# Kernel tuning notes

Hardware: AMD Instinct MI355X
Metric: run time of the kernel (lower is better)

Reference implementation:

```python
import jax, jax.numpy as jnp
import numpy as np

N_USERS = 200_000
N_ITEMS = 100_000
EMB = 64
N_EDGES = 5_000_000
N_LAYERS = 3


def setup_inputs() -> dict:
    key = jax.random.key(0)
    k1, k2, k3, k4, k5 = jax.random.split(key, 5)
    emb_user = jax.random.normal(k1, (N_USERS, EMB), dtype=jnp.float32) * 0.1
    emb_item = jax.random.normal(k2, (N_ITEMS, EMB), dtype=jnp.float32) * 0.1
    n_nodes = N_USERS + N_ITEMS
    edge_row = jax.random.randint(k3, (N_EDGES,), 0, n_nodes, dtype=jnp.int32)
    edge_col = jax.random.randint(k4, (N_EDGES,), 0, n_nodes, dtype=jnp.int32)
    # normalized adjacency values (positive, < 1), stand-in for D^-1/2 A D^-1/2
    edge_val = jax.random.uniform(k5, (N_EDGES,), dtype=jnp.float32)
    return {"emb_user": emb_user, "emb_item": emb_item,
            "edge_val": edge_val, "edge_row": edge_row, "edge_col": edge_col}


def reference(emb_user, emb_item, edge_val, edge_row, edge_col):
    n_users = emb_user.shape[0]
    n_nodes = n_users + emb_item.shape[0]
    # 0th-layer embedding matrix: cat(user, item)  [N, D]
    x = jnp.concatenate([emb_user, emb_item], axis=0)
    layers = [x]
    for _ in range(N_LAYERS):
        # SpMM: out[r] += val * x[c] for each edge (r, c)
        x = jax.ops.segment_sum(edge_val[:, None] * x[edge_col], edge_row,
                                num_segments=n_nodes)
        layers.append(x)
    # layer combination: mean over all layers
    agg = jnp.mean(jnp.stack(layers, axis=0), axis=0)
    return agg[:n_users], agg[n_users:]
```

## Files before the change

### kernel.cpp

```cpp
#include <hip/hip_runtime.h>

#define N_USERS 200000
#define N_ITEMS 100000
#define N_NODES 300000
#define EMB     64
#define N_EDGES 5000000

typedef float f32x4 __attribute__((ext_vector_type(4)));
typedef _Float16 f16;
typedef f16 f16x4 __attribute__((ext_vector_type(4)));

struct alignas(8) SRec { unsigned int rc; float val; };

#define BSHIFT 10
#define BROWS  (1 << BSHIFT)
#define NBUCK  ((N_NODES + BROWS - 1) >> BSHIFT)
#define CAP    20000
#define BIN_CHUNK 16384
#define COLMASK 0x7FFFFu
#define INIT_BLOCKS 2048

__global__ __launch_bounds__(256) void fused_init_bin_kernel(
    const float* __restrict__ user, const float* __restrict__ item,
    f16* __restrict__ x0,
    const int4* __restrict__ row4, const int4* __restrict__ col4,
    const float4* __restrict__ val4,
    int* __restrict__ bcursor, SRec* __restrict__ stage, int bin_blocks)
{
    int t = threadIdx.x;
    if ((int)blockIdx.x < bin_blocks) {
        __shared__ int hist[NBUCK];
        __shared__ int base_[NBUCK];
        const int Q = N_EDGES / 4;
        long q0 = (long)blockIdx.x * (BIN_CHUNK / 4);

        for (int k = t; k < NBUCK; k += 256) hist[k] = 0;
        __syncthreads();

        int4 ra[16];
        const bool full = (q0 + (BIN_CHUNK / 4) <= Q);
        if (full) {
            #pragma unroll
            for (int k = 0; k < 16; ++k)
                ra[k] = row4[q0 + k * 256 + t];
            #pragma unroll
            for (int k = 0; k < 16; ++k) {
                atomicAdd(&hist[ra[k].x >> BSHIFT], 1);
                atomicAdd(&hist[ra[k].y >> BSHIFT], 1);
                atomicAdd(&hist[ra[k].z >> BSHIFT], 1);
                atomicAdd(&hist[ra[k].w >> BSHIFT], 1);
            }
        } else {
            #pragma unroll
            for (int k = 0; k < 16; ++k) {
                long q = q0 + k * 256 + t;
                if (q < Q) {
                    ra[k] = row4[q];
                    atomicAdd(&hist[ra[k].x >> BSHIFT], 1);
                    atomicAdd(&hist[ra[k].y >> BSHIFT], 1);
                    atomicAdd(&hist[ra[k].z >> BSHIFT], 1);
                    atomicAdd(&hist[ra[k].w >> BSHIFT], 1);
                }
            }
        }
        __syncthreads();
        for (int k = t; k < NBUCK; k += 256) {
            int h = hist[k];
            base_[k] = h ? atomicAdd(&bcursor[k], h) : 0;
            hist[k] = 0;
        }
        __syncthreads();
        #pragma unroll
        for (int g = 0; g < 4; ++g) {
            int4 c4[4]; float4 v4[4];
            #pragma unroll
            for (int j = 0; j < 4; ++j) {
                long q = q0 + (g * 4 + j) * 256 + t;
                if (q < Q) { c4[j] = col4[q]; v4[j] = val4[q]; }
            }
            #pragma unroll
            for (int j = 0; j < 4; ++j) {
                long q = q0 + (g * 4 + j) * 256 + t;
                if (q < Q) {
                    int4 r = ra[g * 4 + j];
                    int   rr[4] = {r.x, r.y, r.z, r.w};
                    int   cc[4] = {c4[j].x, c4[j].y, c4[j].z, c4[j].w};
                    float vv[4] = {v4[j].x, v4[j].y, v4[j].z, v4[j].w};
                    #pragma unroll
                    for (int m = 0; m < 4; ++m) {
                        int b   = rr[m] >> BSHIFT;
                        int pos = base_[b] + atomicAdd(&hist[b], 1);
                        SRec s;
                        s.rc  = ((unsigned)(rr[m] & (BROWS - 1)) << 19)
                              | (unsigned)cc[m];
                        s.val = vv[m];
                        stage[(size_t)b * CAP + pos] = s;
                    }
                }
            }
        }
    } else {
        const int nu4 = N_USERS * EMB / 4;
        const int nt4 = N_NODES * EMB / 4;
        int i0 = ((int)blockIdx.x - bin_blocks) * 256 + t;
        const int stride = INIT_BLOCKS * 256;
        for (int i = i0; i < nt4; i += stride) {
            float4 vv = (i < nu4) ? reinterpret_cast<const float4*>(user)[i]
                                  : reinterpret_cast<const float4*>(item)[i - nu4];
            f16x4 hx = {(f16)vv.x, (f16)vv.y, (f16)vv.z, (f16)vv.w};
            reinterpret_cast<f16x4*>(x0)[i] = hx;
        }
    }
}

__global__ __launch_bounds__(1024) void bucket_scan_scatter_kernel(
    const SRec* __restrict__ stage, const int* __restrict__ bsize,
    int* __restrict__ start, int* __restrict__ pcol, f16* __restrict__ pval)
{
    __shared__ int sizes[NBUCK];
    __shared__ int cur[BROWS];
    __shared__ int sc[1024];
    __shared__ int lcol[CAP];
    __shared__ f16 lval[CAP];
    __shared__ int sbase;

    int b    = blockIdx.x;
    int t    = threadIdx.x;
    int row0 = b << BSHIFT;
    int rows = N_NODES - row0; if (rows > BROWS) rows = BROWS;

    if (t < NBUCK) sizes[t] = bsize[t];
    cur[t] = 0;
    __syncthreads();
    if (t == 0) {
        int s = 0;
        for (int k = 0; k < b; ++k) s += sizes[k];
        sbase = s;
    }
    __syncthreads();
    const int  base = sbase;
    const int  size = sizes[b];
    const SRec* seg = stage + (size_t)b * CAP;

    for (int e = t; e < size; e += 1024)
        atomicAdd(&cur[seg[e].rc >> 19], 1);
    __syncthreads();

    int a = cur[t];
    sc[t] = a;
    __syncthreads();
    for (int ofs = 1; ofs < 1024; ofs <<= 1) {
        int v = (t >= ofs) ? sc[t - ofs] : 0;
        __syncthreads();
        sc[t] += v;
        __syncthreads();
    }
    int excl = sc[t] - a;
    cur[t] = excl;
    if (t < rows) start[row0 + t] = base + excl;
    if (b == NBUCK - 1 && t == 0) start[N_NODES] = N_EDGES;
    __syncthreads();

    for (int e = t; e < size; e += 1024) {
        SRec srec = seg[e];
        int idx = atomicAdd(&cur[srec.rc >> 19], 1);
        lcol[idx] = (int)(srec.rc & COLMASK);
        lval[idx] = (f16)srec.val;
    }
    __syncthreads();

    for (int i = t; i < size; i += 1024) pcol[base + i] = lcol[i];
    for (int i = t; i < size; i += 1024) pval[base + i] = lval[i];
}

__global__ __launch_bounds__(256, 4) void spmm_csr_kernel(
    const f16* __restrict__ x, const int* __restrict__ pcol,
    const f16* __restrict__ pval, const int* __restrict__ start,
    f16* __restrict__ y,
    const f16* __restrict__ xa, const f16* __restrict__ xb,
    float* __restrict__ out, int mode)
{
    int g = blockIdx.x * (256 / 16) + (threadIdx.x >> 4);
    if (g >= N_NODES) return;
    const int lane16 = threadIdx.x & 15;
    const int d      = lane16 * 4;
    const int gbase  = threadIdx.x & 48;

    int beg = start[g];
    int end = start[g + 1];
    float4 acc = {0.f, 0.f, 0.f, 0.f};

    for (int jb = beg; jb < end; jb += 16) {
        int   mycol = 0; float myval = 0.f;
        if (jb + lane16 < end) {
            mycol = pcol[jb + lane16];
            myval = (float)pval[jb + lane16];
        }

        int   cols[16];
        float vals[16];
        #pragma unroll
        for (int k = 0; k < 16; ++k) {
            cols[k] = __shfl(mycol, gbase + k, 64);
            vals[k] = __shfl(myval, gbase + k, 64);
        }

        f16x4 xv[16];
        #pragma unroll
        for (int k = 0; k < 16; ++k) {
            xv[k] = *reinterpret_cast<const f16x4*>(
                x + (size_t)cols[k] * EMB + d);
        }

        #pragma unroll
        for (int k = 0; k < 16; ++k) {
            acc.x += vals[k] * (float)xv[k].x;
            acc.y += vals[k] * (float)xv[k].y;
            acc.z += vals[k] * (float)xv[k].z;
            acc.w += vals[k] * (float)xv[k].w;
        }
    }

    const size_t rofs = (size_t)g * EMB + d;
    if (mode == 0) {
        f16x4 hy = {(f16)acc.x, (f16)acc.y, (f16)acc.z, (f16)acc.w};
        *reinterpret_cast<f16x4*>(y + rofs) = hy;
    } else {
        f16x4 v0 = *reinterpret_cast<const f16x4*>(xa + rofs);
        f16x4 v1 = *reinterpret_cast<const f16x4*>(xb + rofs);
        f16x4 v2 = *reinterpret_cast<const f16x4*>(x  + rofs);
        f32x4 o;
        o.x = 0.25f * ((float)v0.x + (float)v1.x + (float)v2.x + acc.x);
        o.y = 0.25f * ((float)v0.y + (float)v1.y + (float)v2.y + acc.y);
        o.z = 0.25f * ((float)v0.z + (float)v1.z + (float)v2.z + acc.z);
        o.w = 0.25f * ((float)v0.w + (float)v1.w + (float)v2.w + acc.w);
        __builtin_nontemporal_store(o, reinterpret_cast<f32x4*>(out + rofs));
    }
}

__global__ __launch_bounds__(256) void init_kernel(
    const float* __restrict__ user, const float* __restrict__ item,
    float* __restrict__ x, float* __restrict__ out)
{
    const int nu4 = N_USERS * EMB / 4;
    const int nt4 = N_NODES * EMB / 4;
    int i = blockIdx.x * blockDim.x + threadIdx.x;
    if (i >= nt4) return;
    float4 v = (i < nu4) ? reinterpret_cast<const float4*>(user)[i]
                         : reinterpret_cast<const float4*>(item)[i - nu4];
    reinterpret_cast<float4*>(x)[i]   = v;
    reinterpret_cast<float4*>(out)[i] = v;
}

__global__ __launch_bounds__(256) void spmm_atomic_kernel(
    const float* __restrict__ x, const float* __restrict__ val,
    const int* __restrict__ row, const int* __restrict__ col,
    float* __restrict__ y)
{
    int t = blockIdx.x * blockDim.x + threadIdx.x;
    int e = t >> 4;
    if (e >= N_EDGES) return;
    int d = (t & 15) * 4;
    int   r = row[e];
    int   c = col[e];
    float v = val[e];
    float4 xv = *reinterpret_cast<const float4*>(x + c * EMB + d);
    float* yp = y + r * EMB + d;
    unsafeAtomicAdd(yp + 0, v * xv.x);
    unsafeAtomicAdd(yp + 1, v * xv.y);
    unsafeAtomicAdd(yp + 2, v * xv.z);
    unsafeAtomicAdd(yp + 3, v * xv.w);
}

__global__ __launch_bounds__(256) void addscale_kernel(
    const float* __restrict__ xl, float* __restrict__ out, float scale)
{
    const int nt4 = N_NODES * EMB / 4;
    int i = blockIdx.x * blockDim.x + threadIdx.x;
    if (i >= nt4) return;
    float4 a = reinterpret_cast<float4*>(out)[i];
    float4 b = reinterpret_cast<const float4*>(xl)[i];
    a.x = (a.x + b.x) * scale;
    a.y = (a.y + b.y) * scale;
    a.z = (a.z + b.z) * scale;
    a.w = (a.w + b.w) * scale;
    reinterpret_cast<float4*>(out)[i] = a;
}

extern "C" void kernel_launch(void* const* d_in, const int* in_sizes, int n_in,
                              void* d_out, int out_size, void* d_ws, size_t ws_size,
                              hipStream_t stream) {
    const float* emb_user = (const float*)d_in[0];
    const float* emb_item = (const float*)d_in[1];
    const float* edge_val = (const float*)d_in[2];
    const int*   edge_row = (const int*)d_in[3];
    const int*   edge_col = (const int*)d_in[4];
    float* out = (float*)d_out;

    const size_t node_elems = (size_t)N_NODES * EMB;
    char* ws = (char*)d_ws;

    const size_t off_bufA    = 0;
    const size_t off_bufB    = off_bufA + node_elems * sizeof(float);
    const size_t off_pcol    = off_bufB + node_elems * sizeof(float);
    const size_t off_pval    = off_pcol + (size_t)N_EDGES * sizeof(int);
    const size_t off_start   = off_pval + (size_t)N_EDGES * sizeof(f16);
    const size_t off_bcursor = off_start + (N_NODES + 4) * sizeof(int);
    const size_t needed      = off_bcursor + (NBUCK + 4) * sizeof(int);

    const int nt4       = N_NODES * EMB / 4;
    const int el_blocks = (nt4 + 255) / 256;
    const int e_blocks  = (N_EDGES + 255) / 256;

    static_assert((size_t)NBUCK * CAP * sizeof(SRec) <= (size_t)N_NODES * EMB * sizeof(float),
                  "stage must fit in bufB region");

    if (ws_size >= needed) {
        f16*  x0buf   = (f16*) (ws + off_bufA);
        f16*  x2buf   = (f16*) (ws + off_bufA) + node_elems;
        f16*  x1buf   = (f16*) (ws + off_bufB);
        int*  pcol    = (int*) (ws + off_pcol);
        f16*  pval    = (f16*) (ws + off_pval);
        int*  start   = (int*) (ws + off_start);
        int*  bcursor = (int*) (ws + off_bcursor);
        SRec* stage   = (SRec*)(ws + off_bufB);

        hipMemsetAsync(bcursor, 0, (NBUCK + 4) * sizeof(int), stream);

        const int bin_blocks = (N_EDGES + BIN_CHUNK - 1) / BIN_CHUNK;
        fused_init_bin_kernel<<<bin_blocks + INIT_BLOCKS, 256, 0, stream>>>(
            emb_user, emb_item, x0buf,
            (const int4*)edge_row, (const int4*)edge_col, (const float4*)edge_val,
            bcursor, stage, bin_blocks);

        bucket_scan_scatter_kernel<<<NBUCK, 1024, 0, stream>>>(
            stage, bcursor, start, pcol, pval);

        const int row_blocks = (N_NODES + 15) / 16;
        spmm_csr_kernel<<<row_blocks, 256, 0, stream>>>(
            x0buf, pcol, pval, start, x1buf, nullptr, nullptr, nullptr, 0);
        spmm_csr_kernel<<<row_blocks, 256, 0, stream>>>(
            x1buf, pcol, pval, start, x2buf, nullptr, nullptr, nullptr, 0);
        spmm_csr_kernel<<<row_blocks, 256, 0, stream>>>(
            x2buf, pcol, pval, start, nullptr, x0buf, x1buf, out, 1);
    } else {
        float* fbufA = (float*)(ws + off_bufA);
        float* fbufB = (float*)(ws + off_bufB);
        init_kernel<<<el_blocks, 256, 0, stream>>>(emb_user, emb_item, fbufA, out);
        const int ew_blocks = (N_EDGES * 16 + 255) / 256;
        float* cur = fbufA;
        float* nxt = fbufB;
        for (int layer = 0; layer < 3; ++layer) {
            hipMemsetAsync(nxt, 0, node_elems * sizeof(float), stream);
            spmm_atomic_kernel<<<ew_blocks, 256, 0, stream>>>(
                cur, edge_val, edge_row, edge_col, nxt);
            addscale_kernel<<<el_blocks, 256, 0, stream>>>(
                nxt, out, (layer == 2) ? 0.25f : 1.0f);
            float* tmp = cur; cur = nxt; nxt = tmp;
        }
    }
}
```

Baseline: 550.0 us.

## Use smaller 256-row buckets with padded CSR segments and per-row counts

Shrinks the bucket size from 1024 to 256 rows and gives each bucket a fixed padded slot of CAP entries in the CSR arrays. This removes the serial prefix sum over bucket sizes, and it makes the scatter kernel run many more, smaller 256-thread blocks with less shared memory each. Because segments are no longer contiguous, a 16-bit per-row count array is added and the SpMM reads beg+cnt instead of start[g+1]. The trade-off is a larger padded CSR footprint and overflow risk if any bucket exceeds 5120 edges. With about 4267 edges expected per bucket, that margin is tight.

```diff
diff --git a/kernel.cpp b/kernel.cpp
--- a/kernel.cpp
+++ b/kernel.cpp
@@ -12,10 +12,10 @@
 
 struct alignas(8) SRec { unsigned int rc; float val; };
 
-#define BSHIFT 10
+#define BSHIFT 8
 #define BROWS  (1 << BSHIFT)
 #define NBUCK  ((N_NODES + BROWS - 1) >> BSHIFT)
-#define CAP    20000
+#define CAP    5120
 #define BIN_CHUNK 16384
 #define COLMASK 0x7FFFFu
 #define INIT_BLOCKS 2048
@@ -113,43 +113,36 @@
     }
 }
 
-__global__ __launch_bounds__(1024) void bucket_scan_scatter_kernel(
+__global__ __launch_bounds__(256) void bucket_scan_scatter_kernel(
     const SRec* __restrict__ stage, const int* __restrict__ bsize,
-    int* __restrict__ start, int* __restrict__ pcol, f16* __restrict__ pval)
-{
-    __shared__ int sizes[NBUCK];
+    int* __restrict__ start, unsigned short* __restrict__ cnt16,
+    int* __restrict__ pcol, f16* __restrict__ pval)
+{
     __shared__ int cur[BROWS];
-    __shared__ int sc[1024];
+    __shared__ int sc[256];
     __shared__ int lcol[CAP];
     __shared__ f16 lval[CAP];
-    __shared__ int sbase;
 
     int b    = blockIdx.x;
     int t    = threadIdx.x;
     int row0 = b << BSHIFT;
     int rows = N_NODES - row0; if (rows > BROWS) rows = BROWS;
 
-    if (t < NBUCK) sizes[t] = bsize[t];
+    const int  size = bsize[b];
+    const int  base = b * CAP;
+    const SRec* seg = stage + (size_t)b * CAP;
+
     cur[t] = 0;
     __syncthreads();
-    if (t == 0) {
-        int s = 0;
-        for (int k = 0; k < b; ++k) s += sizes[k];
-        sbase = s;
-    }
-    __syncthreads();
-    const int  base = sbase;
-    const int  size = sizes[b];
-    const SRec* seg = stage + (size_t)b * CAP;
-
-    for (int e = t; e < size; e += 1024)
+
+    for (int e = t; e < size; e += 256)
         atomicAdd(&cur[seg[e].rc >> 19], 1);
     __syncthreads();
 
     int a = cur[t];
     sc[t] = a;
     __syncthreads();
-    for (int ofs = 1; ofs < 1024; ofs <<= 1) {
+    for (int ofs = 1; ofs < 256; ofs <<= 1) {
         int v = (t >= ofs) ? sc[t - ofs] : 0;
         __syncthreads();
         sc[t] += v;
@@ -157,11 +150,13 @@
     }
     int excl = sc[t] - a;
     cur[t] = excl;
-    if (t < rows) start[row0 + t] = base + excl;
-    if (b == NBUCK - 1 && t == 0) start[N_NODES] = N_EDGES;
-    __syncthreads();
-
-    for (int e = t; e < size; e += 1024) {
+    if (t < rows) {
+        start[row0 + t] = base + excl;
+        cnt16[row0 + t] = (unsigned short)a;
+    }
+    __syncthreads();
+
+    for (int e = t; e < size; e += 256) {
         SRec srec = seg[e];
         int idx = atomicAdd(&cur[srec.rc >> 19], 1);
         lcol[idx] = (int)(srec.rc & COLMASK);
@@ -169,13 +164,14 @@
     }
     __syncthreads();
 
-    for (int i = t; i < size; i += 1024) pcol[base + i] = lcol[i];
-    for (int i = t; i < size; i += 1024) pval[base + i] = lval[i];
+    for (int i = t; i < size; i += 256) pcol[base + i] = lcol[i];
+    for (int i = t; i < size; i += 256) pval[base + i] = lval[i];
 }
 
 __global__ __launch_bounds__(256, 4) void spmm_csr_kernel(
     const f16* __restrict__ x, const int* __restrict__ pcol,
     const f16* __restrict__ pval, const int* __restrict__ start,
+    const unsigned short* __restrict__ cnt16,
     f16* __restrict__ y,
     const f16* __restrict__ xa, const f16* __restrict__ xb,
     float* __restrict__ out, int mode)
@@ -187,7 +183,7 @@
     const int gbase  = threadIdx.x & 48;
 
     int beg = start[g];
-    int end = start[g + 1];
+    int end = beg + cnt16[g];
     float4 acc = {0.f, 0.f, 0.f, 0.f};
 
     for (int jb = beg; jb < end; jb += 16) {
@@ -303,9 +299,10 @@
     const size_t off_bufA    = 0;
     const size_t off_bufB    = off_bufA + node_elems * sizeof(float);
     const size_t off_pcol    = off_bufB + node_elems * sizeof(float);
-    const size_t off_pval    = off_pcol + (size_t)N_EDGES * sizeof(int);
-    const size_t off_start   = off_pval + (size_t)N_EDGES * sizeof(f16);
-    const size_t off_bcursor = off_start + (N_NODES + 4) * sizeof(int);
+    const size_t off_pval    = off_pcol + (size_t)NBUCK * CAP * sizeof(int);
+    const size_t off_start   = off_pval + (size_t)NBUCK * CAP * sizeof(f16);
+    const size_t off_cnt16   = off_start + (N_NODES + 4) * sizeof(int);
+    const size_t off_bcursor = off_cnt16 + (N_NODES + 4) * sizeof(unsigned short);
     const size_t needed      = off_bcursor + (NBUCK + 4) * sizeof(int);
 
     const int nt4       = N_NODES * EMB / 4;
@@ -322,6 +319,7 @@
         int*  pcol    = (int*) (ws + off_pcol);
         f16*  pval    = (f16*) (ws + off_pval);
         int*  start   = (int*) (ws + off_start);
+        unsigned short* cnt16 = (unsigned short*)(ws + off_cnt16);
         int*  bcursor = (int*) (ws + off_bcursor);
         SRec* stage   = (SRec*)(ws + off_bufB);
 
@@ -333,16 +331,16 @@
             (const int4*)edge_row, (const int4*)edge_col, (const float4*)edge_val,
             bcursor, stage, bin_blocks);
 
-        bucket_scan_scatter_kernel<<<NBUCK, 1024, 0, stream>>>(
-            stage, bcursor, start, pcol, pval);
+        bucket_scan_scatter_kernel<<<NBUCK, 256, 0, stream>>>(
+            stage, bcursor, start, cnt16, pcol, pval);
 
         const int row_blocks = (N_NODES + 15) / 16;
         spmm_csr_kernel<<<row_blocks, 256, 0, stream>>>(
-            x0buf, pcol, pval, start, x1buf, nullptr, nullptr, nullptr, 0);
+            x0buf, pcol, pval, start, cnt16, x1buf, nullptr, nullptr, nullptr, 0);
         spmm_csr_kernel<<<row_blocks, 256, 0, stream>>>(
-            x1buf, pcol, pval, start, x2buf, nullptr, nullptr, nullptr, 0);
+            x1buf, pcol, pval, start, cnt16, x2buf, nullptr, nullptr, nullptr, 0);
         spmm_csr_kernel<<<row_blocks, 256, 0, stream>>>(
-            x2buf, pcol, pval, start, nullptr, x0buf, x1buf, out, 1);
+            x2buf, pcol, pval, start, cnt16, nullptr, x0buf, x1buf, out, 1);
     } else {
         float* fbufA = (float*)(ws + off_bufA);
         float* fbufB = (float*)(ws + off_bufB);
```

Result: slower. 569.5 us (+3.5%).
